# Kernel optimization log

Measured on AMD Instinct MI355X. Metric: run time of the kernel, lower is better.

Reference implementation:

```python
import jax, jax.numpy as jnp
import numpy as np

HIDDEN = 2560
N_HEADS = 8
N_KV = 4
HEAD_DIM = 256
SLIDING_WINDOW = 512
SOFTCAP = 50.0
EPS = 1e-6
ROPE_BASE = 10000.0


def setup_inputs() -> dict:
    key = jax.random.key(0)
    ks = jax.random.split(key, 6)
    B, L = 2, 2048
    x = jax.random.normal(ks[0], (B, L, HIDDEN), dtype=jnp.float32)
    mask = jnp.zeros((1, 1, L, L), dtype=jnp.float32)  # additive attention mask
    s = 0.02
    q_w = jax.random.normal(ks[1], (N_HEADS * HEAD_DIM, HIDDEN), dtype=jnp.float32) * s
    k_w = jax.random.normal(ks[2], (N_KV * HEAD_DIM, HIDDEN), dtype=jnp.float32) * s
    v_w = jax.random.normal(ks[3], (N_KV * HEAD_DIM, HIDDEN), dtype=jnp.float32) * s
    o_w = jax.random.normal(ks[4], (HIDDEN, N_HEADS * HEAD_DIM), dtype=jnp.float32) * s
    # Gemma RMSNorm scale initialized to zero (acts as (1 + w))
    q_norm_w = jnp.zeros((HEAD_DIM,), dtype=jnp.float32)
    k_norm_w = jnp.zeros((HEAD_DIM,), dtype=jnp.float32)
    return {"x": x, "mask": mask, "q_w": q_w, "k_w": k_w, "v_w": v_w,
            "o_w": o_w, "q_norm_w": q_norm_w, "k_norm_w": k_norm_w}


def rms_norm(x, w):
    x32 = x.astype(jnp.float32)
    normed = x32 * jax.lax.rsqrt(jnp.mean(x32 * x32, axis=-1, keepdims=True) + EPS)
    return (normed * (1.0 + w)).astype(x.dtype)


def rope_cos_sin(L):
    inv_freq = 1.0 / (ROPE_BASE ** (np.arange(0, HEAD_DIM, 2, dtype=np.float32) / HEAD_DIM))
    t = np.arange(L, dtype=np.float32)
    freqs = np.outer(t, inv_freq)                      # (L, D/2)
    emb = np.concatenate([freqs, freqs], axis=-1)      # (L, D)
    return jnp.asarray(np.cos(emb)), jnp.asarray(np.sin(emb))


def apply_rope(x, cos, sin):
    # x: (B, H, L, D); cos/sin: (L, D)
    half = x.shape[-1] // 2
    rot = jnp.concatenate([-x[..., half:], x[..., :half]], axis=-1)
    return x * cos[None, None] + rot * sin[None, None]


def reference(x, mask, q_w, k_w, v_w, o_w, q_norm_w, k_norm_w):
    B, L, _ = x.shape
    q = (x @ q_w.T).reshape(B, L, N_HEADS, HEAD_DIM).transpose(0, 2, 1, 3)   # (B,Hq,L,D)
    k = (x @ k_w.T).reshape(B, L, N_KV, HEAD_DIM).transpose(0, 2, 1, 3)      # (B,Hkv,L,D)
    v = (x @ v_w.T).reshape(B, L, N_KV, HEAD_DIM).transpose(0, 2, 1, 3)
    q = rms_norm(q, q_norm_w)
    k = rms_norm(k, k_norm_w)
    cos, sin = rope_cos_sin(L)
    q = apply_rope(q, cos, sin)
    k = apply_rope(k, cos, sin)
    groups = N_HEADS // N_KV
    if groups > 1:  # GQA repeat_interleave on head dim
        k = jnp.repeat(k, groups, axis=1)
        v = jnp.repeat(v, groups, axis=1)
    scale = HEAD_DIM ** (-0.5)
    attn_w = jnp.einsum('bhqd,bhkd->bhqk', q, k) * scale
    attn_w = SOFTCAP * jnp.tanh(attn_w / SOFTCAP)
    attn_w = attn_w + mask
    kv_len = attn_w.shape[-1]
    if kv_len > SLIDING_WINDOW:
        # module keeps only the LAST sliding_window key columns for all rows
        col_ok = jnp.arange(kv_len) >= (kv_len - SLIDING_WINDOW)
        attn_w = jnp.where(col_ok[None, None, None, :], attn_w, -jnp.inf)
    attn_w = jax.nn.softmax(attn_w.astype(jnp.float32), axis=-1).astype(q.dtype)
    out = jnp.einsum('bhqk,bhkd->bhqd', attn_w, v)
    out = out.transpose(0, 2, 1, 3).reshape(B, L, N_HEADS * HEAD_DIM)
    return out @ o_w.T
```

## Files before the change

### kernel.cpp

```cpp
#include <hip/hip_runtime.h>
#include <hip/hip_bf16.h>
#include <cstdint>
#include <cmath>


using bf16 = __hip_bfloat16;
typedef __attribute__((ext_vector_type(8))) short short8;
typedef __attribute__((ext_vector_type(4))) float f32x4;

__device__ inline void gl_lds16(const void* g, void* l) {
  __builtin_amdgcn_global_load_lds(
      (const __attribute__((address_space(1))) unsigned int*)g,
      (__attribute__((address_space(3))) unsigned int*)l, 16, 0, 0);
}

__global__ __launch_bounds__(256)
void cvt_bf16(const float4* __restrict__ in, __hip_bfloat162* __restrict__ out,
              int n4) {
  const int i = blockIdx.x * 256 + threadIdx.x;
  if (i < n4) {
    const float4 v = in[i];
    __hip_bfloat162 lo, hi;
    lo.x = __float2bfloat16(v.x); lo.y = __float2bfloat16(v.y);
    hi.x = __float2bfloat16(v.z); hi.y = __float2bfloat16(v.w);
    out[2 * i] = lo;
    out[2 * i + 1] = hi;
  }
}

template <int EPI>
__global__ __launch_bounds__(512, 2)
void gemm256(const bf16* __restrict__ A, const bf16* __restrict__ B,
             void* __restrict__ C0, void* __restrict__ C1,
             void* __restrict__ C2, int K, int lda, int ldb, int ldc) {
  extern __shared__ short lds[];
  short* As = lds;
  short* Bs = lds + 32768;
  const int t = threadIdx.x;
  const int lane = t & 63;
  const int wid = t >> 6, wm = wid >> 2, wn = wid & 3;
  const int m16 = lane & 15, quad = lane >> 4;
  const int brow = blockIdx.y * 256, bcol = blockIdx.x * 256;

  const int srow = t >> 2;
  const int scol = ((t & 3) ^ ((srow >> 1) & 3)) * 8;
  const bf16* gA0 = A + (size_t)(brow + srow) * lda + scol;
  const bf16* gA1 = A + (size_t)(brow + 128 + srow) * lda + scol;
  const bf16* gB0 = B + (size_t)(bcol + srow) * ldb + scol;
  const bf16* gB1 = B + (size_t)(bcol + 128 + srow) * ldb + scol;
  const int dst = t * 8;

  const int rbA = (wm * 128 + m16) * 32;
  const int rbB = (wn * 64 + m16) * 32;
  const int sw = (quad ^ ((m16 >> 1) & 3)) * 8;

  f32x4 acc[8][4] = {};
  short8 a[8], b[4];

  const int nkt = K >> 5;
#pragma unroll
  for (int p = 0; p < 3; ++p) {
    const int o = p * 32;
    short* sa = As + p * 8192;
    short* sb = Bs + p * 8192;
    gl_lds16(gA0 + o, sa + dst);
    gl_lds16(gA1 + o, sa + 4096 + dst);
    gl_lds16(gB0 + o, sb + dst);
    gl_lds16(gB1 + o, sb + 4096 + dst);
  }
  asm volatile("s_waitcnt vmcnt(8)" ::: "memory");
  asm volatile("s_barrier" ::: "memory");

  for (int kt = 0; kt < nkt; ++kt) {
    const short* Ab = As + (kt & 3) * 8192;
    const short* Bb = Bs + (kt & 3) * 8192;
    const bool pre = (kt + 3) < nkt;
    const int po = (kt + 3) << 5;
    short* pa = As + ((kt + 3) & 3) * 8192;
    short* pb = Bs + ((kt + 3) & 3) * 8192;

#pragma unroll
    for (int nj = 0; nj < 4; ++nj)
      b[nj] = *(const short8*)&Bb[rbB + nj * 512 + sw];
#pragma unroll
    for (int mi = 0; mi < 8; ++mi)
      a[mi] = *(const short8*)&Ab[rbA + mi * 512 + sw];
    if (pre) {
      gl_lds16(gA0 + po, pa + dst);
      gl_lds16(gA1 + po, pa + 4096 + dst);
      gl_lds16(gB0 + po, pb + dst);
      gl_lds16(gB1 + po, pb + 4096 + dst);
    }
    __builtin_amdgcn_s_setprio(1);
#pragma unroll
    for (int mi = 0; mi < 8; ++mi)
#pragma unroll
      for (int nj = 0; nj < 4; ++nj)
        acc[mi][nj] = __builtin_amdgcn_mfma_f32_16x16x32_bf16(
            a[mi], b[nj], acc[mi][nj], 0, 0, 0);
    __builtin_amdgcn_s_setprio(0);
    if (kt + 4 <= nkt) {
      asm volatile("s_waitcnt vmcnt(8) lgkmcnt(0)" ::: "memory");
    } else if (kt + 3 == nkt) {
      asm volatile("s_waitcnt vmcnt(4) lgkmcnt(0)" ::: "memory");
    } else if (kt + 2 == nkt) {
      asm volatile("s_waitcnt vmcnt(0) lgkmcnt(0)" ::: "memory");
    } else {
      asm volatile("s_waitcnt lgkmcnt(0)" ::: "memory");
    }
    asm volatile("s_barrier" ::: "memory");
  }

  const int row0 = brow + wm * 128 + quad * 4;
  const int col0 = bcol + wn * 64 + m16;
#pragma unroll
  for (int mi = 0; mi < 8; ++mi) {
#pragma unroll
    for (int ni = 0; ni < 4; ++ni) {
      const int col = col0 + ni * 16;
#pragma unroll
      for (int r = 0; r < 4; ++r) {
        const int row = row0 + mi * 16 + r;
        const float v = acc[mi][ni][r];
        if constexpr (EPI == 0) {
          if (col < 2048) {
            ((bf16*)C0)[(size_t)row * 2048 + col] = __float2bfloat16(v);
          } else if (col < 3072) {
            ((bf16*)C1)[(size_t)row * 1024 + (col - 2048)] = __float2bfloat16(v);
          } else {
            const int b2 = row >> 11;
            ((bf16*)C2)[((size_t)(b2 * 1024 + (col - 3072))) * 2048 +
                        (row & 2047)] = __float2bfloat16(v);
          }
        } else {
          ((float*)C0)[(size_t)row * ldc + col] = v;
        }
      }
    }
  }
}

template <int EPI>
__global__ __launch_bounds__(256)
void gemm(const bf16* __restrict__ A, const bf16* __restrict__ B,
          void* __restrict__ Cv, int K, int lda, int ldb, int ldc,
          long sAh, long sBh, long sCh, float cscale) {
  __shared__ short As[4096];
  __shared__ short Bs[4096];
  const int t = threadIdx.x, lane = t & 63, w = t >> 6;
  const int zh = blockIdx.z;
  A += (size_t)zh * sAh;
  B += (size_t)(zh >> 1) * sBh;
  const size_t coff = (size_t)zh * sCh;
  const int blockRow = blockIdx.y * 128, blockCol = blockIdx.x * 128;

  const int e = t * 8;
  const int srow = t >> 2, scol = (t & 3) * 8;
  const bf16* gA0 = A + (size_t)(blockRow + srow) * lda + scol;
  const bf16* gA1 = gA0 + (size_t)64 * lda;
  const bf16* gB0 = B + (size_t)(blockCol + srow) * ldb + scol;
  const bf16* gB1 = gB0 + (size_t)64 * ldb;

  const int wm = w >> 1, wn = w & 1;
  const int quad = lane >> 4, m16 = lane & 15;
  f32x4 acc[4][4] = {};

  for (int kt = 0; kt < K; kt += 32) {
    __syncthreads();
    gl_lds16(gA0 + kt, &As[e]);
    gl_lds16(gA1 + kt, &As[e + 2048]);
    gl_lds16(gB0 + kt, &Bs[e]);
    gl_lds16(gB1 + kt, &Bs[e + 2048]);
    __syncthreads();
    short8 af[4], bfr[4];
#pragma unroll
    for (int i = 0; i < 4; ++i)
      af[i] = *(const short8*)&As[(wm * 64 + i * 16 + m16) * 32 + quad * 8];
#pragma unroll
    for (int j = 0; j < 4; ++j)
      bfr[j] = *(const short8*)&Bs[(wn * 64 + j * 16 + m16) * 32 + quad * 8];
#pragma unroll
    for (int i = 0; i < 4; ++i)
#pragma unroll
      for (int j = 0; j < 4; ++j)
        acc[i][j] = __builtin_amdgcn_mfma_f32_16x16x32_bf16(af[i], bfr[j],
                                                            acc[i][j], 0, 0, 0);
  }

#pragma unroll
  for (int i = 0; i < 4; ++i) {
#pragma unroll
    for (int j = 0; j < 4; ++j) {
      const int gcol = blockCol + wn * 64 + j * 16 + m16;
#pragma unroll
      for (int r = 0; r < 4; ++r) {
        const int grow = blockRow + wm * 64 + i * 16 + quad * 4 + r;
        float v = acc[i][j][r] * cscale;
        if constexpr (EPI == 1) {
          const float y = v * 0.02f;
          const float ee = __expf(-2.0f * fabsf(y));
          v = copysignf(50.0f * (1.0f - ee) / (1.0f + ee), y);
          ((float*)Cv)[coff + (size_t)grow * ldc + gcol] = v;
        } else {
          ((bf16*)Cv)[coff + (size_t)grow * ldc + gcol] = __float2bfloat16(v);
        }
      }
    }
  }
}

__global__ __launch_bounds__(256)
void norm_rope(bf16* __restrict__ qk, const float* __restrict__ nw, int hmod) {
  const int seg = blockIdx.x * 4 + (threadIdx.x >> 6);
  const int lane = threadIdx.x & 63;
  bf16* p = qk + (size_t)seg * 256;
  float x0 = __bfloat162float(p[lane]);
  float x1 = __bfloat162float(p[lane + 64]);
  float x2 = __bfloat162float(p[lane + 128]);
  float x3 = __bfloat162float(p[lane + 192]);
  float ss = x0 * x0 + x1 * x1 + x2 * x2 + x3 * x3;
#pragma unroll
  for (int o = 32; o; o >>= 1) ss += __shfl_xor(ss, o);
  const float r = rsqrtf(ss * (1.0f / 256.0f) + 1e-6f);
  const float n0 = x0 * r * (1.0f + nw[lane]);
  const float n1 = x1 * r * (1.0f + nw[lane + 64]);
  const float n2 = x2 * r * (1.0f + nw[lane + 128]);
  const float n3 = x3 * r * (1.0f + nw[lane + 192]);
  const int l = (seg / hmod) & 2047;
  const float kf = -9.210340371976184f / 128.0f;
  float c0, s0, c1, s1;
  sincosf((float)l * expf(kf * (float)lane), &s0, &c0);
  sincosf((float)l * expf(kf * (float)(lane + 64)), &s1, &c1);
  p[lane]       = __float2bfloat16(n0 * c0 - n2 * s0);
  p[lane + 128] = __float2bfloat16(n2 * c0 + n0 * s0);
  p[lane + 64]  = __float2bfloat16(n1 * c1 - n3 * s1);
  p[lane + 192] = __float2bfloat16(n3 * c1 + n1 * s1);
}

__global__ __launch_bounds__(256)
void softmax_k(float* __restrict__ S) {
  const int row = blockIdx.x * 4 + (threadIdx.x >> 6);
  const int lane = threadIdx.x & 63;
  float* rowp = S + (size_t)row * 512;
  const float4 a = ((const float4*)rowp)[lane];
  const float4 b = ((const float4*)rowp)[lane + 64];
  float mx = fmaxf(fmaxf(fmaxf(a.x, a.y), fmaxf(a.z, a.w)),
                   fmaxf(fmaxf(b.x, b.y), fmaxf(b.z, b.w)));
#pragma unroll
  for (int o = 32; o; o >>= 1) mx = fmaxf(mx, __shfl_xor(mx, o));
  float e0 = expf(a.x - mx), e1 = expf(a.y - mx);
  float e2 = expf(a.z - mx), e3 = expf(a.w - mx);
  float f0 = expf(b.x - mx), f1 = expf(b.y - mx);
  float f2 = expf(b.z - mx), f3 = expf(b.w - mx);
  float sum = e0 + e1 + e2 + e3 + f0 + f1 + f2 + f3;
#pragma unroll
  for (int o = 32; o; o >>= 1) sum += __shfl_xor(sum, o);
  const float inv = 1.0f / sum;
  bf16* p0 = (bf16*)rowp + lane * 4;
  p0[0] = __float2bfloat16(e0 * inv);
  p0[1] = __float2bfloat16(e1 * inv);
  p0[2] = __float2bfloat16(e2 * inv);
  p0[3] = __float2bfloat16(e3 * inv);
  bf16* p1 = p0 + 256;
  p1[0] = __float2bfloat16(f0 * inv);
  p1[1] = __float2bfloat16(f1 * inv);
  p1[2] = __float2bfloat16(f2 * inv);
  p1[3] = __float2bfloat16(f3 * inv);
}

extern "C" void kernel_launch(void* const* d_in, const int* in_sizes, int n_in,
                              void* d_out, int out_size, void* d_ws, size_t ws_size,
                              hipStream_t stream) {
  const float* x    = (const float*)d_in[0];
  const float* q_w  = (const float*)d_in[2];
  const float* k_w  = (const float*)d_in[3];
  const float* v_w  = (const float*)d_in[4];
  const float* o_w  = (const float*)d_in[5];
  const float* q_nw = (const float*)d_in[6];
  const float* k_nw = (const float*)d_in[7];
  float* out = (float*)d_out;

  char* wsb = (char*)d_ws;
  bf16* xb    = (bf16*)(wsb);
  float* sc   = (float*)(wsb);
  bf16* qkvwb = (bf16*)(wsb + 20971520);
  bf16* owb   = qkvwb;
  bf16* kwb   = (bf16*)(wsb + 31457280);
  bf16* vwb   = (bf16*)(wsb + 36700160);
  bf16* q_ws  = (bf16*)(wsb + 41943040);
  bf16* k_ws  = (bf16*)(wsb + 58720256);
  bf16* vT    = (bf16*)(wsb + 67108864);
  bf16* attn  = q_ws;

  static bool attr_set = false;
  if (!attr_set) {
    (void)hipFuncSetAttribute(reinterpret_cast<const void*>(&gemm256<0>),
                              hipFuncAttributeMaxDynamicSharedMemorySize, 131072);
    (void)hipFuncSetAttribute(reinterpret_cast<const void*>(&gemm256<1>),
                              hipFuncAttributeMaxDynamicSharedMemorySize, 131072);
    attr_set = true;
  }

  dim3 blk(256);
  cvt_bf16<<<dim3(10240), blk, 0, stream>>>((const float4*)x,   (__hip_bfloat162*)xb,    2621440);
  cvt_bf16<<<dim3(5120),  blk, 0, stream>>>((const float4*)q_w, (__hip_bfloat162*)qkvwb, 1310720);
  cvt_bf16<<<dim3(2560),  blk, 0, stream>>>((const float4*)k_w, (__hip_bfloat162*)kwb,   655360);
  cvt_bf16<<<dim3(2560),  blk, 0, stream>>>((const float4*)v_w, (__hip_bfloat162*)vwb,   655360);
  gemm256<0><<<dim3(16, 16), dim3(512), 131072, stream>>>(
      xb, qkvwb, (void*)q_ws, (void*)k_ws, (void*)vT, 2560, 2560, 2560, 0);
  cvt_bf16<<<dim3(5120), blk, 0, stream>>>((const float4*)o_w, (__hip_bfloat162*)owb, 1310720);
  norm_rope<<<dim3(8192), blk, 0, stream>>>(q_ws, q_nw, 8);
  norm_rope<<<dim3(4096), blk, 0, stream>>>(k_ws, k_nw, 4);
  for (int b = 0; b < 2; ++b) {
    for (int c = 0; c < 2; ++c) {
      gemm<1><<<dim3(4, 16, 4), blk, 0, stream>>>(
          q_ws + (size_t)b * 4194304 + c * 1024,
          k_ws + (size_t)b * 2097152 + 1572864 + c * 512,
          (void*)sc, 256, 2048, 1024, 512,
          256L, 256L, 1048576L, 1.0f / 16.0f);
      softmax_k<<<dim3(2048), blk, 0, stream>>>(sc);
      gemm<0><<<dim3(2, 16, 4), blk, 0, stream>>>(
          (const bf16*)sc,
          vT + (size_t)b * 2097152 + (size_t)c * 1048576 + 1536,
          (void*)(attn + (size_t)b * 4194304 + c * 1024), 512, 1024, 2048, 2048,
          2097152L, 524288L, 256L, 1.0f);
    }
  }
  gemm256<1><<<dim3(10, 16), dim3(512), 131072, stream>>>(
      attn, owb, (void*)out, nullptr, nullptr, 2048, 2048, 2048, 2560);
}
```

Before: 480.4 us.

## Double-buffer A fragments across k-steps and merge input conversion kernels

```diff
diff --git a/kernel.cpp b/kernel.cpp
--- a/kernel.cpp
+++ b/kernel.cpp
@@ -12,6 +12,31 @@
   __builtin_amdgcn_global_load_lds(
       (const __attribute__((address_space(1))) unsigned int*)g,
       (__attribute__((address_space(3))) unsigned int*)l, 16, 0, 0);
+}
+
+__global__ __launch_bounds__(256)
+void cvt_qkvx(const float4* __restrict__ x, const float4* __restrict__ qw,
+              const float4* __restrict__ kw, const float4* __restrict__ vw,
+              __hip_bfloat162* __restrict__ xb, __hip_bfloat162* __restrict__ qkvwb) {
+  const int blk = blockIdx.x;
+  const float4* src;
+  __hip_bfloat162* dstb;
+  int i;
+  if (blk < 10240) {
+    src = x;    dstb = xb;             i = blk * 256 + threadIdx.x;
+  } else if (blk < 15360) {
+    src = qw;   dstb = qkvwb;          i = (blk - 10240) * 256 + threadIdx.x;
+  } else if (blk < 17920) {
+    src = kw;   dstb = qkvwb + 2621440; i = (blk - 15360) * 256 + threadIdx.x;
+  } else {
+    src = vw;   dstb = qkvwb + 3932160; i = (blk - 17920) * 256 + threadIdx.x;
+  }
+  const float4 v = src[i];
+  __hip_bfloat162 lo, hi;
+  lo.x = __float2bfloat16(v.x); lo.y = __float2bfloat16(v.y);
+  hi.x = __float2bfloat16(v.z); hi.y = __float2bfloat16(v.w);
+  dstb[2 * i] = lo;
+  dstb[2 * i + 1] = hi;
 }
 
 __global__ __launch_bounds__(256)
@@ -55,7 +80,7 @@
   const int sw = (quad ^ ((m16 >> 1) & 3)) * 8;
 
   f32x4 acc[8][4] = {};
-  short8 a[8], b[4];
+  short8 aA[8], aB[8];
 
   const int nkt = K >> 5;
 #pragma unroll
@@ -68,47 +93,54 @@
     gl_lds16(gB0 + o, sb + dst);
     gl_lds16(gB1 + o, sb + 4096 + dst);
   }
-  asm volatile("s_waitcnt vmcnt(8)" ::: "memory");
+  asm volatile("s_waitcnt vmcnt(4)" ::: "memory");
   asm volatile("s_barrier" ::: "memory");
-
-  for (int kt = 0; kt < nkt; ++kt) {
-    const short* Ab = As + (kt & 3) * 8192;
-    const short* Bb = Bs + (kt & 3) * 8192;
-    const bool pre = (kt + 3) < nkt;
-    const int po = (kt + 3) << 5;
-    short* pa = As + ((kt + 3) & 3) * 8192;
-    short* pb = Bs + ((kt + 3) & 3) * 8192;
-
-#pragma unroll
-    for (int nj = 0; nj < 4; ++nj)
-      b[nj] = *(const short8*)&Bb[rbB + nj * 512 + sw];
-#pragma unroll
-    for (int mi = 0; mi < 8; ++mi)
-      a[mi] = *(const short8*)&Ab[rbA + mi * 512 + sw];
-    if (pre) {
+#pragma unroll
+  for (int mi = 0; mi < 8; ++mi)
+    aA[mi] = *(const short8*)&As[rbA + mi * 512 + sw];
+
+  auto ITER = [&](int j, short8 (&ac)[8], short8 (&an)[8]) {
+    if (j + 3 < nkt) {
+      const int po = (j + 3) << 5;
+      short* pa = As + ((j + 3) & 3) * 8192;
+      short* pb = Bs + ((j + 3) & 3) * 8192;
       gl_lds16(gA0 + po, pa + dst);
       gl_lds16(gA1 + po, pa + 4096 + dst);
       gl_lds16(gB0 + po, pb + dst);
       gl_lds16(gB1 + po, pb + 4096 + dst);
     }
+    const short* Bb = Bs + (j & 3) * 8192;
+    short8 b[4];
+#pragma unroll
+    for (int nj = 0; nj < 4; ++nj)
+      b[nj] = *(const short8*)&Bb[rbB + nj * 512 + sw];
+    if (j + 1 < nkt) {
+      const short* An = As + ((j + 1) & 3) * 8192;
+#pragma unroll
+      for (int mi = 0; mi < 8; ++mi)
+        an[mi] = *(const short8*)&An[rbA + mi * 512 + sw];
+    }
     __builtin_amdgcn_s_setprio(1);
 #pragma unroll
-    for (int mi = 0; mi < 8; ++mi)
-#pragma unroll
-      for (int nj = 0; nj < 4; ++nj)
+    for (int nj = 0; nj < 4; ++nj)
+#pragma unroll
+      for (int mi = 0; mi < 8; ++mi)
         acc[mi][nj] = __builtin_amdgcn_mfma_f32_16x16x32_bf16(
-            a[mi], b[nj], acc[mi][nj], 0, 0, 0);
+            ac[mi], b[nj], acc[mi][nj], 0, 0, 0);
     __builtin_amdgcn_s_setprio(0);
-    if (kt + 4 <= nkt) {
-      asm volatile("s_waitcnt vmcnt(8) lgkmcnt(0)" ::: "memory");
-    } else if (kt + 3 == nkt) {
+    if (j + 4 <= nkt) {
       asm volatile("s_waitcnt vmcnt(4) lgkmcnt(0)" ::: "memory");
-    } else if (kt + 2 == nkt) {
+    } else if (j + 3 == nkt) {
       asm volatile("s_waitcnt vmcnt(0) lgkmcnt(0)" ::: "memory");
     } else {
       asm volatile("s_waitcnt lgkmcnt(0)" ::: "memory");
     }
     asm volatile("s_barrier" ::: "memory");
+  };
+
+  for (int kt = 0; kt < nkt; kt += 2) {
+    ITER(kt, aA, aB);
+    ITER(kt + 1, aB, aA);
   }
 
   const int row0 = brow + wm * 128 + quad * 4;
@@ -285,8 +317,6 @@
   float* sc   = (float*)(wsb);
   bf16* qkvwb = (bf16*)(wsb + 20971520);
   bf16* owb   = qkvwb;
-  bf16* kwb   = (bf16*)(wsb + 31457280);
-  bf16* vwb   = (bf16*)(wsb + 36700160);
   bf16* q_ws  = (bf16*)(wsb + 41943040);
   bf16* k_ws  = (bf16*)(wsb + 58720256);
   bf16* vT    = (bf16*)(wsb + 67108864);
@@ -302,10 +332,9 @@
   }
 
   dim3 blk(256);
-  cvt_bf16<<<dim3(10240), blk, 0, stream>>>((const float4*)x,   (__hip_bfloat162*)xb,    2621440);
-  cvt_bf16<<<dim3(5120),  blk, 0, stream>>>((const float4*)q_w, (__hip_bfloat162*)qkvwb, 1310720);
-  cvt_bf16<<<dim3(2560),  blk, 0, stream>>>((const float4*)k_w, (__hip_bfloat162*)kwb,   655360);
-  cvt_bf16<<<dim3(2560),  blk, 0, stream>>>((const float4*)v_w, (__hip_bfloat162*)vwb,   655360);
+  cvt_qkvx<<<dim3(20480), blk, 0, stream>>>(
+      (const float4*)x, (const float4*)q_w, (const float4*)k_w,
+      (const float4*)v_w, (__hip_bfloat162*)xb, (__hip_bfloat162*)qkvwb);
   gemm256<0><<<dim3(16, 16), dim3(512), 131072, stream>>>(
       xb, qkvwb, (void*)q_ws, (void*)k_ws, (void*)vT, 2560, 2560, 2560, 0);
   cvt_bf16<<<dim3(5120), blk, 0, stream>>>((const float4*)o_w, (__hip_bfloat162*)owb, 1310720);
```

New measurement: 477.3 us. No clear change (-0.6%).

## Fuse QK^T, softcap and softmax into one kernel; defer normalization to PV epilogue

Applied to the files above, without the earlier changes.

```diff
diff --git a/kernel.cpp b/kernel.cpp
--- a/kernel.cpp
+++ b/kernel.cpp
@@ -12,6 +12,31 @@
   __builtin_amdgcn_global_load_lds(
       (const __attribute__((address_space(1))) unsigned int*)g,
       (__attribute__((address_space(3))) unsigned int*)l, 16, 0, 0);
+}
+
+__global__ __launch_bounds__(256)
+void cvt_qkvx(const float4* __restrict__ x, const float4* __restrict__ qw,
+              const float4* __restrict__ kw, const float4* __restrict__ vw,
+              __hip_bfloat162* __restrict__ xb, __hip_bfloat162* __restrict__ qkvwb) {
+  const int blk = blockIdx.x;
+  const float4* src;
+  __hip_bfloat162* dstb;
+  int i;
+  if (blk < 10240) {
+    src = x;    dstb = xb;             i = blk * 256 + threadIdx.x;
+  } else if (blk < 15360) {
+    src = qw;   dstb = qkvwb;          i = (blk - 10240) * 256 + threadIdx.x;
+  } else if (blk < 17920) {
+    src = kw;   dstb = qkvwb + 2621440; i = (blk - 15360) * 256 + threadIdx.x;
+  } else {
+    src = vw;   dstb = qkvwb + 3932160; i = (blk - 17920) * 256 + threadIdx.x;
+  }
+  const float4 v = src[i];
+  __hip_bfloat162 lo, hi;
+  lo.x = __float2bfloat16(v.x); lo.y = __float2bfloat16(v.y);
+  hi.x = __float2bfloat16(v.z); hi.y = __float2bfloat16(v.w);
+  dstb[2 * i] = lo;
+  dstb[2 * i + 1] = hi;
 }
 
 __global__ __launch_bounds__(256)
@@ -144,7 +169,8 @@
 __global__ __launch_bounds__(256)
 void gemm(const bf16* __restrict__ A, const bf16* __restrict__ B,
           void* __restrict__ Cv, int K, int lda, int ldb, int ldc,
-          long sAh, long sBh, long sCh, float cscale) {
+          long sAh, long sBh, long sCh, float cscale,
+          const float* __restrict__ rs) {
   __shared__ short As[4096];
   __shared__ short Bs[4096];
   const int t = threadIdx.x, lane = t & 63, w = t >> 6;
@@ -196,17 +222,149 @@
       for (int r = 0; r < 4; ++r) {
         const int grow = blockRow + wm * 64 + i * 16 + quad * 4 + r;
         float v = acc[i][j][r] * cscale;
-        if constexpr (EPI == 1) {
-          const float y = v * 0.02f;
-          const float ee = __expf(-2.0f * fabsf(y));
-          v = copysignf(50.0f * (1.0f - ee) / (1.0f + ee), y);
-          ((float*)Cv)[coff + (size_t)grow * ldc + gcol] = v;
+        if constexpr (EPI == 4) {
+          v *= rs[zh * 2048 + grow];
+          ((bf16*)Cv)[coff + (size_t)grow * ldc + gcol] = __float2bfloat16(v);
         } else {
           ((bf16*)Cv)[coff + (size_t)grow * ldc + gcol] = __float2bfloat16(v);
         }
       }
     }
   }
+}
+
+__global__ __launch_bounds__(512, 2)
+void attn_ss(const bf16* __restrict__ q, const bf16* __restrict__ k,
+             bf16* __restrict__ P, float* __restrict__ invs) {
+  extern __shared__ short lds[];
+  short* Qs = lds;
+  short* Ks = lds + 2048;
+  const int t = threadIdx.x, lane = t & 63;
+  const int wid = t >> 6, wm = wid >> 2, wn = wid & 3;
+  const int m16 = lane & 15, quad = lane >> 4;
+  const int mt = blockIdx.x;
+  const int h = blockIdx.y;
+
+  const int srow = t >> 2;
+  const int scol = ((t & 3) ^ ((srow >> 1) & 3)) * 8;
+  const bf16* gQ = q + (size_t)(mt * 64 + srow) * 2048 + h * 256 + scol;
+  const bf16* gK = k + (size_t)(1536 + srow) * 1024 + (h >> 1) * 256 + scol;
+  const int dst = t * 8;
+
+  const int rbA = (wm * 32 + m16) * 32;
+  const int rbB = (wn * 128 + m16) * 32;
+  const int sw = (quad ^ ((m16 >> 1) & 3)) * 8;
+
+  f32x4 acc[2][8] = {};
+  for (int kt = 0; kt < 256; kt += 32) {
+    __syncthreads();
+    if (t < 256) gl_lds16(gQ + kt, &Qs[dst]);
+    gl_lds16(gK + kt, &Ks[dst]);
+    gl_lds16(gK + kt + (size_t)128 * 1024, &Ks[4096 + dst]);
+    gl_lds16(gK + kt + (size_t)256 * 1024, &Ks[8192 + dst]);
+    gl_lds16(gK + kt + (size_t)384 * 1024, &Ks[12288 + dst]);
+    __syncthreads();
+    short8 aq[2], bk[8];
+#pragma unroll
+    for (int mi = 0; mi < 2; ++mi)
+      aq[mi] = *(const short8*)&Qs[rbA + mi * 512 + sw];
+#pragma unroll
+    for (int nj = 0; nj < 8; ++nj)
+      bk[nj] = *(const short8*)&Ks[rbB + nj * 512 + sw];
+#pragma unroll
+    for (int mi = 0; mi < 2; ++mi)
+#pragma unroll
+      for (int nj = 0; nj < 8; ++nj)
+        acc[mi][nj] = __builtin_amdgcn_mfma_f32_16x16x32_bf16(
+            aq[mi], bk[nj], acc[mi][nj], 0, 0, 0);
+  }
+
+#pragma unroll
+  for (int mi = 0; mi < 2; ++mi)
+#pragma unroll
+    for (int nj = 0; nj < 8; ++nj)
+#pragma unroll
+      for (int r = 0; r < 4; ++r) {
+        const float y = acc[mi][nj][r] * (0.02f / 16.0f);
+        const float ee = __expf(-2.0f * fabsf(y));
+        acc[mi][nj][r] = copysignf(50.0f * (1.0f - ee) / (1.0f + ee), y);
+      }
+
+  float* red = (float*)lds;
+
+  float mrow[2][4];
+#pragma unroll
+  for (int mi = 0; mi < 2; ++mi)
+#pragma unroll
+    for (int r = 0; r < 4; ++r) {
+      float m = acc[mi][0][r];
+#pragma unroll
+      for (int nj = 1; nj < 8; ++nj) m = fmaxf(m, acc[mi][nj][r]);
+#pragma unroll
+      for (int o = 1; o < 16; o <<= 1) m = fmaxf(m, __shfl_xor(m, o));
+      mrow[mi][r] = m;
+    }
+  __syncthreads();
+  if (m16 == 0) {
+#pragma unroll
+    for (int mi = 0; mi < 2; ++mi)
+#pragma unroll
+      for (int r = 0; r < 4; ++r)
+        red[wn * 64 + wm * 32 + mi * 16 + quad * 4 + r] = mrow[mi][r];
+  }
+  __syncthreads();
+#pragma unroll
+  for (int mi = 0; mi < 2; ++mi)
+#pragma unroll
+    for (int r = 0; r < 4; ++r) {
+      const int row = wm * 32 + mi * 16 + quad * 4 + r;
+      mrow[mi][r] = fmaxf(fmaxf(red[row], red[64 + row]),
+                          fmaxf(red[128 + row], red[192 + row]));
+    }
+
+  float srow_[2][4] = {};
+#pragma unroll
+  for (int mi = 0; mi < 2; ++mi)
+#pragma unroll
+    for (int nj = 0; nj < 8; ++nj)
+#pragma unroll
+      for (int r = 0; r < 4; ++r) {
+        const float e = __expf(acc[mi][nj][r] - mrow[mi][r]);
+        acc[mi][nj][r] = e;
+        srow_[mi][r] += e;
+      }
+#pragma unroll
+  for (int mi = 0; mi < 2; ++mi)
+#pragma unroll
+    for (int r = 0; r < 4; ++r)
+#pragma unroll
+      for (int o = 1; o < 16; o <<= 1)
+        srow_[mi][r] += __shfl_xor(srow_[mi][r], o);
+  __syncthreads();
+  if (m16 == 0) {
+#pragma unroll
+    for (int mi = 0; mi < 2; ++mi)
+#pragma unroll
+      for (int r = 0; r < 4; ++r)
+        red[wn * 64 + wm * 32 + mi * 16 + quad * 4 + r] = srow_[mi][r];
+  }
+  __syncthreads();
+
+  bf16* Pout = P + (size_t)h * 1048576 + (size_t)(mt * 64) * 512;
+#pragma unroll
+  for (int mi = 0; mi < 2; ++mi)
+#pragma unroll
+    for (int r = 0; r < 4; ++r) {
+      const int row = wm * 32 + mi * 16 + quad * 4 + r;
+      const float sum = red[row] + red[64 + row] + red[128 + row] +
+                        red[192 + row];
+      if (wn == 0 && m16 == 0)
+        invs[h * 2048 + mt * 64 + row] = 1.0f / sum;
+#pragma unroll
+      for (int nj = 0; nj < 8; ++nj)
+        Pout[(size_t)row * 512 + wn * 128 + nj * 16 + m16] =
+            __float2bfloat16(acc[mi][nj][r]);
+    }
 }
 
 __global__ __launch_bounds__(256)
@@ -237,37 +395,6 @@
   p[lane + 192] = __float2bfloat16(n3 * c1 + n1 * s1);
 }
 
-__global__ __launch_bounds__(256)
-void softmax_k(float* __restrict__ S) {
-  const int row = blockIdx.x * 4 + (threadIdx.x >> 6);
-  const int lane = threadIdx.x & 63;
-  float* rowp = S + (size_t)row * 512;
-  const float4 a = ((const float4*)rowp)[lane];
-  const float4 b = ((const float4*)rowp)[lane + 64];
-  float mx = fmaxf(fmaxf(fmaxf(a.x, a.y), fmaxf(a.z, a.w)),
-                   fmaxf(fmaxf(b.x, b.y), fmaxf(b.z, b.w)));
-#pragma unroll
-  for (int o = 32; o; o >>= 1) mx = fmaxf(mx, __shfl_xor(mx, o));
-  float e0 = expf(a.x - mx), e1 = expf(a.y - mx);
-  float e2 = expf(a.z - mx), e3 = expf(a.w - mx);
-  float f0 = expf(b.x - mx), f1 = expf(b.y - mx);
-  float f2 = expf(b.z - mx), f3 = expf(b.w - mx);
-  float sum = e0 + e1 + e2 + e3 + f0 + f1 + f2 + f3;
-#pragma unroll
-  for (int o = 32; o; o >>= 1) sum += __shfl_xor(sum, o);
-  const float inv = 1.0f / sum;
-  bf16* p0 = (bf16*)rowp + lane * 4;
-  p0[0] = __float2bfloat16(e0 * inv);
-  p0[1] = __float2bfloat16(e1 * inv);
-  p0[2] = __float2bfloat16(e2 * inv);
-  p0[3] = __float2bfloat16(e3 * inv);
-  bf16* p1 = p0 + 256;
-  p1[0] = __float2bfloat16(f0 * inv);
-  p1[1] = __float2bfloat16(f1 * inv);
-  p1[2] = __float2bfloat16(f2 * inv);
-  p1[3] = __float2bfloat16(f3 * inv);
-}
-
 extern "C" void kernel_launch(void* const* d_in, const int* in_sizes, int n_in,
                               void* d_out, int out_size, void* d_ws, size_t ws_size,
                               hipStream_t stream) {
@@ -282,11 +409,10 @@
 
   char* wsb = (char*)d_ws;
   bf16* xb    = (bf16*)(wsb);
-  float* sc   = (float*)(wsb);
+  bf16* P     = (bf16*)(wsb);
+  float* invs = (float*)(wsb + 16777216);
   bf16* qkvwb = (bf16*)(wsb + 20971520);
   bf16* owb   = qkvwb;
-  bf16* kwb   = (bf16*)(wsb + 31457280);
-  bf16* vwb   = (bf16*)(wsb + 36700160);
   bf16* q_ws  = (bf16*)(wsb + 41943040);
   bf16* k_ws  = (bf16*)(wsb + 58720256);
   bf16* vT    = (bf16*)(wsb + 67108864);
@@ -302,29 +428,21 @@
   }
 
   dim3 blk(256);
-  cvt_bf16<<<dim3(10240), blk, 0, stream>>>((const float4*)x,   (__hip_bfloat162*)xb,    2621440);
-  cvt_bf16<<<dim3(5120),  blk, 0, stream>>>((const float4*)q_w, (__hip_bfloat162*)qkvwb, 1310720);
-  cvt_bf16<<<dim3(2560),  blk, 0, stream>>>((const float4*)k_w, (__hip_bfloat162*)kwb,   655360);
-  cvt_bf16<<<dim3(2560),  blk, 0, stream>>>((const float4*)v_w, (__hip_bfloat162*)vwb,   655360);
+  cvt_qkvx<<<dim3(20480), blk, 0, stream>>>(
+      (const float4*)x, (const float4*)q_w, (const float4*)k_w,
+      (const float4*)v_w, (__hip_bfloat162*)xb, (__hip_bfloat162*)qkvwb);
   gemm256<0><<<dim3(16, 16), dim3(512), 131072, stream>>>(
       xb, qkvwb, (void*)q_ws, (void*)k_ws, (void*)vT, 2560, 2560, 2560, 0);
   cvt_bf16<<<dim3(5120), blk, 0, stream>>>((const float4*)o_w, (__hip_bfloat162*)owb, 1310720);
   norm_rope<<<dim3(8192), blk, 0, stream>>>(q_ws, q_nw, 8);
   norm_rope<<<dim3(4096), blk, 0, stream>>>(k_ws, k_nw, 4);
   for (int b = 0; b < 2; ++b) {
-    for (int c = 0; c < 2; ++c) {
-      gemm<1><<<dim3(4, 16, 4), blk, 0, stream>>>(
-          q_ws + (size_t)b * 4194304 + c * 1024,
-          k_ws + (size_t)b * 2097152 + 1572864 + c * 512,
-          (void*)sc, 256, 2048, 1024, 512,
-          256L, 256L, 1048576L, 1.0f / 16.0f);
-      softmax_k<<<dim3(2048), blk, 0, stream>>>(sc);
-      gemm<0><<<dim3(2, 16, 4), blk, 0, stream>>>(
-          (const bf16*)sc,
-          vT + (size_t)b * 2097152 + (size_t)c * 1048576 + 1536,
-          (void*)(attn + (size_t)b * 4194304 + c * 1024), 512, 1024, 2048, 2048,
-          2097152L, 524288L, 256L, 1.0f);
-    }
+    attn_ss<<<dim3(32, 8), dim3(512), 36864, stream>>>(
+        q_ws + (size_t)b * 4194304, k_ws + (size_t)b * 2097152, P, invs);
+    gemm<4><<<dim3(2, 16, 8), blk, 0, stream>>>(
+        P, vT + (size_t)b * 2097152 + 1536,
+        (void*)(attn + (size_t)b * 4194304), 512, 512, 2048, 2048,
+        1048576L, 524288L, 256L, 1.0f, invs);
   }
   gemm256<1><<<dim3(10, 16), dim3(512), 131072, stream>>>(
       attn, owb, (void*)out, nullptr, nullptr, 2048, 2048, 2048, 2560);
```

Measured after the change: 402.9 us. 1.19x faster.
